# Performance work log

Hardware: AMD Instinct MI355X
Metric: run time of the kernel (lower is better)

Reference implementation:

```python
import jax, jax.numpy as jnp
from jax import lax
import numpy as np

EPS = 1e-8
NUM_ROUTES = 1152  # 32 * 6 * 6
NUM_OBJ = 10
OBJ_DIM = 16
PC_CAPS = 8
PC_CH = 32


def _squash(s, axis=-1):
    sq = jnp.sum(s * s, axis=axis, keepdims=True)
    return (sq / (1.0 + sq)) * s / jnp.sqrt(sq + EPS)


def setup_inputs() -> dict:
    key = jax.random.key(0)
    ks = jax.random.split(key, 12)
    B = 512
    image = jax.random.uniform(ks[0], (B, 1, 28, 28), dtype=jnp.float32)
    label = jax.random.randint(ks[1], (B,), 0, NUM_OBJ)
    conv_w = jax.random.normal(ks[2], (256, 1, 9, 9), dtype=jnp.float32) * 0.05
    conv_b = jnp.zeros((256,), jnp.float32)
    pc_w = jax.random.normal(ks[3], (PC_CAPS, PC_CH, 256, 9, 9), dtype=jnp.float32) * 0.02
    pc_b = jnp.zeros((PC_CAPS, PC_CH), jnp.float32)
    W_route = jax.random.normal(ks[4], (NUM_ROUTES, NUM_OBJ, OBJ_DIM, PC_CAPS), dtype=jnp.float32)
    dec_w1 = jax.random.normal(ks[5], (512, NUM_OBJ * OBJ_DIM), dtype=jnp.float32) * 0.05
    dec_b1 = jnp.zeros((512,), jnp.float32)
    dec_w2 = jax.random.normal(ks[6], (1024, 512), dtype=jnp.float32) * 0.05
    dec_b2 = jnp.zeros((1024,), jnp.float32)
    dec_w3 = jax.random.normal(ks[7], (784, 1024), dtype=jnp.float32) * 0.05
    dec_b3 = jnp.zeros((784,), jnp.float32)
    return {"image": image, "label": label, "conv_w": conv_w, "conv_b": conv_b,
            "pc_w": pc_w, "pc_b": pc_b, "W_route": W_route,
            "dec_w1": dec_w1, "dec_b1": dec_b1, "dec_w2": dec_w2, "dec_b2": dec_b2,
            "dec_w3": dec_w3, "dec_b3": dec_b3}


def reference(image, label, conv_w, conv_b, pc_w, pc_b, W_route,
              dec_w1, dec_b1, dec_w2, dec_b2, dec_w3, dec_b3):
    B = image.shape[0]
    # ConvEncoder: [B,1,28,28] -> [B,256,20,20]
    x = lax.conv_general_dilated(image, conv_w, (1, 1), 'VALID',
                                 dimension_numbers=('NCHW', 'OIHW', 'NCHW'))
    x = jax.nn.relu(x + conv_b[None, :, None, None])
    # PrimaryCaps: 8 parallel convs fused into one conv with 8*32 out channels
    pw = pc_w.reshape(PC_CAPS * PC_CH, 256, 9, 9)
    u = lax.conv_general_dilated(x, pw, (2, 2), 'VALID',
                                 dimension_numbers=('NCHW', 'OIHW', 'NCHW'))
    u = u + pc_b.reshape(-1)[None, :, None, None]  # [B,256,6,6] == stack dim=1 of [B,8,32,6,6]
    # faithful torch .view: [B,8,32,6,6] row-major -> [B,1152,8]
    u = u.reshape(B, NUM_ROUTES, PC_CAPS)
    u = _squash(u, axis=-1)
    # ObjectCaps dynamic routing
    # u_hat[b,r,j,o] = sum_c W[r,j,o,c] * u[b,r,c]
    u_hat = jnp.einsum('rjoc,brc->brjo', W_route, u)  # [B,1152,10,16]
    b_ij = jnp.zeros((B, NUM_ROUTES, NUM_OBJ), u_hat.dtype)
    v = None
    for it in range(3):
        c_ij = jax.nn.softmax(b_ij, axis=2)                  # softmax over capsules j
        s_j = jnp.einsum('brj,brjo->bjo', c_ij, u_hat)       # [B,10,16]
        v = _squash(s_j, axis=-1)
        if it < 2:
            b_ij = b_ij + jnp.einsum('brjo,bjo->brj', u_hat, v)
    obj_vectors = v[..., None]  # [B,10,16,1]
    # safe_norm over dim=2, squeeze(-1)
    y_prob = jnp.sqrt(jnp.sum(v * v, axis=-1) + EPS)  # [B,10]
    # Decoder: mask by label one-hot, MLP to reconstruction
    mask = jax.nn.one_hot(label, NUM_OBJ, dtype=v.dtype)
    masked = (v * mask[:, :, None]).reshape(B, NUM_OBJ * OBJ_DIM)
    h = jax.nn.relu(masked @ dec_w1.T + dec_b1)
    h = jax.nn.relu(h @ dec_w2.T + dec_b2)
    recon = jax.nn.sigmoid(h @ dec_w3.T + dec_b3).reshape(B, 1, 28, 28)
    return obj_vectors, recon, y_prob
```

## Files before the change

### kernel.cpp

```cpp
#include <hip/hip_runtime.h>
#include <hip/hip_bf16.h>

#define EPSF 1e-8f

typedef __attribute__((ext_vector_type(8))) short short8v;
typedef __attribute__((ext_vector_type(4))) float float4v;

static __device__ __forceinline__ unsigned short f2bf_bits(float x)
{
    return __builtin_bit_cast(unsigned short, __float2bfloat16(x));
}

__global__ __launch_bounds__(256) void k_prep(const float* __restrict__ pw,
                                              __hip_bfloat16* __restrict__ Bw2,
                                              const float* __restrict__ img,
                                              const float* __restrict__ cw,
                                              const float* __restrict__ cb,
                                              __hip_bfloat16* __restrict__ xt)
{
    __shared__ alignas(16) char shmem[41472];
    const int bid = blockIdx.x;
    const int t = threadIdx.x;

    if (bid < 256) {
        const int oc = bid;
        unsigned short* wl = (unsigned short*)shmem;
        for (int i = t; i < 20736; i += 256)
            wl[i] = f2bf_bits(pw[(size_t)oc * 20736 + i]);
        __syncthreads();
        const int r16 = oc & 15, nt = (oc >> 4) & 3, wcq = oc >> 6;
        for (int e = t; e < 2592; e += 256) {
            const int kidx = e >> 5, icc = (e >> 2) & 7, slot = e & 3;
            short8v v;
            #pragma unroll
            for (int i = 0; i < 8; ++i)
                v[i] = (short)wl[(icc * 32 + slot * 8 + i) * 81 + kidx];
            const int chunk = ((kidx * 8 + icc) * 4 + wcq) * 4 + nt;
            *(short8v*)(Bw2 + (size_t)chunk * 512 + (slot * 16 + r16) * 8) = v;
        }
        return;
    }

    const int b = bid - 256;
    const int c = t;
    float* simg = (float*)shmem;
    for (int i = c; i < 784; i += 256) simg[i] = img[b * 784 + i];
    float wreg[81];
    const float* wp = cw + c * 81;
    #pragma unroll
    for (int k = 0; k < 81; ++k) wreg[k] = wp[k];
    const float bias = cb[c];
    __syncthreads();

    const int icc = c >> 5, slot = (c >> 3) & 3, ic8 = c & 7;
    char* xbase = (char*)xt + ((size_t)b * 8 + icc) * 25600;

    for (int wg = 0; wg < 5; ++wg) {
        const float* base = &simg[wg * 4];
        float win[9][12];
        #pragma unroll
        for (int r = 0; r < 8; ++r) {
            const float4v* rp = (const float4v*)(base + r * 28);
            float4v A = rp[0], B = rp[1], C = rp[2];
            win[r][0] = A.x; win[r][1] = A.y; win[r][2]  = A.z; win[r][3]  = A.w;
            win[r][4] = B.x; win[r][5] = B.y; win[r][6]  = B.z; win[r][7]  = B.w;
            win[r][8] = C.x; win[r][9] = C.y; win[r][10] = C.z; win[r][11] = C.w;
        }
        #pragma unroll
        for (int h = 0; h < 20; ++h) {
            {
                const int ws = (h + 8) % 9;
                const float4v* rp = (const float4v*)(base + (h + 8) * 28);
                float4v A = rp[0], B = rp[1], C = rp[2];
                win[ws][0] = A.x; win[ws][1] = A.y; win[ws][2]  = A.z; win[ws][3]  = A.w;
                win[ws][4] = B.x; win[ws][5] = B.y; win[ws][6]  = B.z; win[ws][7]  = B.w;
                win[ws][8] = C.x; win[ws][9] = C.y; win[ws][10] = C.z; win[ws][11] = C.w;
            }
            float acc[4] = {bias, bias, bias, bias};
            #pragma unroll
            for (int ky = 0; ky < 9; ++ky) {
                const int rs = (h + ky) % 9;
                #pragma unroll
                for (int kx = 0; kx < 9; ++kx) {
                    const float wv = wreg[ky * 9 + kx];
                    #pragma unroll
                    for (int i = 0; i < 4; ++i)
                        acc[i] = fmaf(win[rs][kx + i], wv, acc[i]);
                }
            }
            #pragma unroll
            for (int i = 0; i < 4; ++i) {
                int w = wg * 4 + i;
                float av = fmaxf(acc[i], 0.f);
                int pos = h * 20 + (w & 1) * 10 + (w >> 1);
                int off = pos * 64 + ((slot ^ ((pos >> 1) & 3)) << 4) + ic8 * 2;
                *(unsigned short*)(xbase + off) = f2bf_bits(av);
            }
        }
    }
}

__device__ __forceinline__ void stage_x(const __hip_bfloat16* __restrict__ xt,
                                        char* dst, int b0, int icc, int t)
{
    const __hip_bfloat16* base0 = xt + ((size_t)(b0    ) * 8 + icc) * 12800;
    const __hip_bfloat16* base1 = xt + ((size_t)(b0 + 1) * 8 + icc) * 12800;
    #pragma unroll
    for (int k = 0; k < 12; ++k) {
        const int unit = t + k * 256;
        const __hip_bfloat16* gp = (unit < 1600) ? (base0 + unit * 8)
                                                 : (base1 + (unit - 1600) * 8);
        __builtin_amdgcn_global_load_lds(
            (const __attribute__((address_space(1))) unsigned int*)gp,
            (__attribute__((address_space(3))) unsigned int*)(dst + unit * 16),
            16, 0, 0);
    }
    if (t < 128) {
        const int unit = 3072 + t;
        const __hip_bfloat16* gp = base1 + (unit - 1600) * 8;
        __builtin_amdgcn_global_load_lds(
            (const __attribute__((address_space(1))) unsigned int*)gp,
            (__attribute__((address_space(3))) unsigned int*)(dst + unit * 16),
            16, 0, 0);
    }
}

__global__ __launch_bounds__(256, 2) void k_conv2(const __hip_bfloat16* __restrict__ xt,
                                                  const __hip_bfloat16* __restrict__ Bw2,
                                                  const float* __restrict__ pcb,
                                                  float* __restrict__ u0,
                                                  float* __restrict__ u1)
{
    const int pair = blockIdx.x >> 1;
    const int ks = blockIdx.x & 1;
    const int b0 = pair * 2;
    const int t = threadIdx.x;
    const int lane = t & 63, wc = t >> 6;
    const int r16 = lane & 15, slot = lane >> 4;

    __shared__ alignas(16) char xs[51200];

    int aimg[5], lc[5];
    #pragma unroll
    for (int mt = 0; mt < 5; ++mt) {
        int grow = mt * 16 + r16;
        int img = (grow >= 36 && grow < 72) ? 1 : 0;
        int hw = (grow < 72) ? (grow - 36 * img) : 0;
        int h = hw / 6, w = hw - h * 6;
        aimg[mt] = img * 25600;
        lc[mt] = 40 * h + w;
    }

    float4v acc[5][4];
    #pragma unroll
    for (int mt = 0; mt < 5; ++mt)
        #pragma unroll
        for (int nt = 0; nt < 4; ++nt)
            acc[mt][nt] = (float4v){0.f, 0.f, 0.f, 0.f};

    for (int i4 = 0; i4 < 4; ++i4) {
        const int icc = ks * 4 + i4;
        __syncthreads();
        stage_x(xt, xs, b0, icc, t);
        __syncthreads();

        const __hip_bfloat16* bp = Bw2 + ((size_t)icc * 4 + wc) * 2048 + lane * 8;

        #pragma unroll 3
        for (int kidx = 0; kidx < 81; ++kidx) {
            int ky = kidx / 9, kx = kidx - ky * 9;
            int scalK = 20 * ky + 10 * (kx & 1) + (kx >> 1);
            short8v a[5];
            #pragma unroll
            for (int mt = 0; mt < 5; ++mt) {
                int pos = lc[mt] + scalK;
                int off = aimg[mt] + pos * 64 + (((slot ^ (pos >> 1)) & 3) << 4);
                a[mt] = *(const short8v*)(xs + off);
            }
            const __hip_bfloat16* bq = bp + (size_t)kidx * 65536;
            short8v bv[4];
            #pragma unroll
            for (int nt = 0; nt < 4; ++nt)
                bv[nt] = *(const short8v*)(bq + nt * 512);
            #pragma unroll
            for (int mt = 0; mt < 5; ++mt)
                #pragma unroll
                for (int nt = 0; nt < 4; ++nt)
                    acc[mt][nt] = __builtin_amdgcn_mfma_f32_16x16x32_bf16(a[mt], bv[nt], acc[mt][nt], 0, 0, 0);
        }
    }

    float* uo = ks ? u1 : u0;
    #pragma unroll
    for (int mt = 0; mt < 5; ++mt) {
        int grow0 = mt * 16 + slot * 4;
        if (grow0 < 72) {
            int img = grow0 >= 36;
            int hwb = grow0 - 36 * img;
            const int b = b0 + img;
            #pragma unroll
            for (int nt = 0; nt < 4; ++nt) {
                int oc = wc * 64 + nt * 16 + r16;
                float pb = ks ? 0.f : pcb[oc];
                float4v v = acc[mt][nt];
                v.x += pb; v.y += pb; v.z += pb; v.w += pb;
                *(float4v*)(uo + (size_t)b * 9216 + oc * 36 + hwb) = v;
            }
        }
    }
}

__global__ __launch_bounds__(256, 2) void k_route3(const float* __restrict__ u0,
                                                   const float* __restrict__ u1,
                                                   const float* __restrict__ W,
                                                   const float* __restrict__ vsum,
                                                   float* __restrict__ spart, int iter)
{
    const int bid = blockIdx.x;
    const int rc = bid % 144;
    const int bc = bid / 144;
    const int r0 = rc * 8;
    const int b0 = bc * 128;
    const int t = threadIdx.x;
    const int oq = t & 3;
    const int img = t >> 2;
    const int bA = b0 + img, bB = bA + 64;

    __shared__ alignas(16) float Wl[10240];
    __shared__ alignas(16) float ul[128 * 68];

    #pragma unroll
    for (int k = 0; k < 10; ++k) {
        int e = t + k * 256;
        int rr = e / 320, rest = e - rr * 320;
        float4v val = *(const float4v*)(W + (size_t)(r0 + rr) * 1280 + rest * 4);
        int es = e ^ ((e >> 3) & 3);
        *(float4v*)(Wl + es * 4) = val;
    }
    #pragma unroll
    for (int k = 0; k < 4; ++k) {
        int e = t + k * 256;
        int im = e >> 3, cap = e & 7;
        size_t gb = (size_t)(b0 + im) * 9216 + rc * 64 + cap * 8;
        const float4v* pA = (const float4v*)(u0 + gb);
        const float4v* pB = (const float4v*)(u1 + gb);
        float4v a = pA[0] + pB[0];
        float4v c = pA[1] + pB[1];
        float sq = a.x * a.x + a.y * a.y + a.z * a.z + a.w * a.w
                 + c.x * c.x + c.y * c.y + c.z * c.z + c.w * c.w;
        float scale = (sq / (1.f + sq)) / sqrtf(sq + EPSF);
        a *= scale; c *= scale;
        *(float4v*)(ul + im * 68 + cap * 8) = a;
        *(float4v*)(ul + im * 68 + cap * 8 + 4) = c;
    }
    __syncthreads();

    float4v accA[10], accB[10];
    #pragma unroll
    for (int j = 0; j < 10; ++j) {
        accA[j] = (float4v){0.f, 0.f, 0.f, 0.f};
        accB[j] = (float4v){0.f, 0.f, 0.f, 0.f};
    }

    const float* upA = ul + img * 68;
    const float* upB = ul + (img + 64) * 68;

    for (int r = 0; r < 8; ++r) {
        float4v uA0 = *(const float4v*)(upA + r * 8);
        float4v uA1 = *(const float4v*)(upA + r * 8 + 4);
        float4v uB0 = *(const float4v*)(upB + r * 8);
        float4v uB1 = *(const float4v*)(upB + r * 8 + 4);
        float4v uhA[10], uhB[10];
        #pragma unroll
        for (int j = 0; j < 10; ++j) {
            #pragma unroll
            for (int oo = 0; oo < 4; ++oo) {
                int un = r * 320 + j * 32 + oq * 8 + oo * 2;
                int i0 = un ^ oq;
                int i1 = i0 ^ 1;
                float4v wlo = *(const float4v*)(Wl + i0 * 4);
                float4v whi = *(const float4v*)(Wl + i1 * 4);
                uhA[j][oo] = wlo.x * uA0.x + wlo.y * uA0.y + wlo.z * uA0.z + wlo.w * uA0.w
                           + whi.x * uA1.x + whi.y * uA1.y + whi.z * uA1.z + whi.w * uA1.w;
                uhB[j][oo] = wlo.x * uB0.x + wlo.y * uB0.y + wlo.z * uB0.z + wlo.w * uB0.w
                           + whi.x * uB1.x + whi.y * uB1.y + whi.z * uB1.z + whi.w * uB1.w;
            }
        }
        if (iter > 0) {
            #pragma unroll 2
            for (int half = 0; half < 2; ++half) {
                const int b = half ? bB : bA;
                float4v* uh = half ? uhB : uhA;
                float4v* acc = half ? accB : accA;
                float q[10];
                #pragma unroll
                for (int j = 0; j < 10; ++j) {
                    float4v vj = *(const float4v*)(vsum + (size_t)b * 160 + j * 16 + oq * 4);
                    float qp = uh[j].x * vj.x + uh[j].y * vj.y
                             + uh[j].z * vj.z + uh[j].w * vj.w;
                    qp += __shfl_xor(qp, 1);
                    qp += __shfl_xor(qp, 2);
                    q[j] = qp;
                }
                float mx = q[0];
                #pragma unroll
                for (int j = 1; j < 10; ++j) mx = fmaxf(mx, q[j]);
                float ssum = 0.f;
                float c[10];
                #pragma unroll
                for (int j = 0; j < 10; ++j) { c[j] = __expf(q[j] - mx); ssum += c[j]; }
                float inv = 1.f / ssum;
                #pragma unroll
                for (int j = 0; j < 10; ++j) acc[j] += (c[j] * inv) * uh[j];
            }
        } else {
            #pragma unroll
            for (int j = 0; j < 10; ++j) {
                accA[j] += 0.1f * uhA[j];
                accB[j] += 0.1f * uhB[j];
            }
        }
    }

    float* dstA = spart + ((size_t)rc * 512 + bA) * 160 + oq * 4;
    float* dstB = spart + ((size_t)rc * 512 + bB) * 160 + oq * 4;
    #pragma unroll
    for (int j = 0; j < 10; ++j) {
        *(float4v*)(dstA + j * 16) = accA[j];
        *(float4v*)(dstB + j * 16) = accB[j];
    }
}

__global__ void k_finish(const float* __restrict__ spart, float* __restrict__ vsum,
                         float* __restrict__ obj, float* __restrict__ yprob, int iter)
{
    const int b = blockIdx.x, t = threadIdx.x;
    if (t < 160) {
        const float* sp = spart + (size_t)b * 160 + t;
        float sv = 0.f;
        #pragma unroll 8
        for (int rc = 0; rc < 144; ++rc)
            sv += sp[(size_t)rc * 81920];
        float sq = sv * sv;
        sq += __shfl_xor(sq, 1); sq += __shfl_xor(sq, 2);
        sq += __shfl_xor(sq, 4); sq += __shfl_xor(sq, 8);
        float v = sv * (sq / (1.f + sq)) / sqrtf(sq + EPSF);
        float pv = (iter > 0) ? vsum[b * 160 + t] : 0.f;
        vsum[b * 160 + t] = pv + v;
        if (iter == 2) {
            obj[b * 160 + t] = v;
            float vv = v * v;
            vv += __shfl_xor(vv, 1); vv += __shfl_xor(vv, 2);
            vv += __shfl_xor(vv, 4); vv += __shfl_xor(vv, 8);
            if ((t & 15) == 0) yprob[b * 10 + (t >> 4)] = sqrtf(vv + EPSF);
        }
    }
}

__global__ __launch_bounds__(256) void k_mlp1g(const float* __restrict__ obj,
                                               const int* __restrict__ label,
                                               const float* __restrict__ w1,
                                               const float* __restrict__ b1,
                                               float* __restrict__ h1)
{
    const int b0 = blockIdx.x * 8;
    const int t = threadIdx.x;
    __shared__ float vl[8][16];
    __shared__ int labs[8];
    if (t < 8) labs[t] = label[b0 + t];
    __syncthreads();
    if (t < 128) {
        int m = t >> 4, o = t & 15;
        vl[m][o] = obj[(size_t)(b0 + m) * 160 + labs[m] * 16 + o];
    }
    __syncthreads();
    #pragma unroll 2
    for (int nn = 0; nn < 2; ++nn) {
        const int n = t + nn * 256;
        const float bs = b1[n];
        #pragma unroll
        for (int m = 0; m < 8; ++m) {
            const float4v* wp = (const float4v*)(w1 + (size_t)n * 160 + labs[m] * 16);
            float4v w0 = wp[0], w1v = wp[1], w2 = wp[2], w3 = wp[3];
            float q = bs;
            q += vl[m][0]  * w0.x  + vl[m][1]  * w0.y  + vl[m][2]  * w0.z  + vl[m][3]  * w0.w;
            q += vl[m][4]  * w1v.x + vl[m][5]  * w1v.y + vl[m][6]  * w1v.z + vl[m][7]  * w1v.w;
            q += vl[m][8]  * w2.x  + vl[m][9]  * w2.y  + vl[m][10] * w2.z  + vl[m][11] * w2.w;
            q += vl[m][12] * w3.x  + vl[m][13] * w3.y  + vl[m][14] * w3.z  + vl[m][15] * w3.w;
            h1[(size_t)(b0 + m) * 512 + n] = fmaxf(q, 0.f);
        }
    }
}

__global__ void k_mlp(const float* __restrict__ A, const float* __restrict__ Wt,
                      const float* __restrict__ bias, float* __restrict__ C,
                      int N, int K, int act)
{
    const int m0 = blockIdx.x * 32;
    const int n0 = blockIdx.y * 32;
    const int t  = threadIdx.x;
    const int tn = t & 31, tg = t >> 5;
    __shared__ float As[32][33];
    __shared__ float Ws[32][33];
    float acc[4] = {0.f, 0.f, 0.f, 0.f};
    for (int k0 = 0; k0 < K; k0 += 32) {
        __syncthreads();
        for (int idx = t; idx < 1024; idx += 256) {
            int rr = idx >> 5, kk = idx & 31;
            As[rr][kk] = A[(size_t)(m0 + rr) * K + k0 + kk];
            int n = n0 + rr;
            Ws[rr][kk] = (n < N) ? Wt[(size_t)n * K + k0 + kk] : 0.f;
        }
        __syncthreads();
        #pragma unroll 8
        for (int kk = 0; kk < 32; ++kk) {
            float bv = Ws[tn][kk];
            #pragma unroll
            for (int i = 0; i < 4; ++i)
                acc[i] += As[tg * 4 + i][kk] * bv;
        }
    }
    int n = n0 + tn;
    if (n < N) {
        float bs = bias[n];
        #pragma unroll
        for (int i = 0; i < 4; ++i) {
            float vv = acc[i] + bs;
            vv = (act == 0) ? fmaxf(vv, 0.f) : 1.f / (1.f + expf(-vv));
            C[(size_t)(m0 + tg * 4 + i) * N + n] = vv;
        }
    }
}

extern "C" void kernel_launch(void* const* d_in, const int* in_sizes, int n_in,
                              void* d_out, int out_size, void* d_ws, size_t ws_size,
                              hipStream_t stream)
{
    const float* image  = (const float*)d_in[0];
    const int*   label  = (const int*)  d_in[1];
    const float* conv_w = (const float*)d_in[2];
    const float* conv_b = (const float*)d_in[3];
    const float* pc_w   = (const float*)d_in[4];
    const float* pc_b   = (const float*)d_in[5];
    const float* Wrt    = (const float*)d_in[6];
    const float* dw1 = (const float*)d_in[7];
    const float* db1 = (const float*)d_in[8];
    const float* dw2 = (const float*)d_in[9];
    const float* db2 = (const float*)d_in[10];
    const float* dw3 = (const float*)d_in[11];
    const float* db3 = (const float*)d_in[12];
    float* out = (float*)d_out;

    char* p = (char*)d_ws;
    __hip_bfloat16* xt  = (__hip_bfloat16*)p; p += 104857600;
    float* u      = (float*)p; p += 18874368;
    float* u1     = (float*)p; p += 18874368;
    __hip_bfloat16* Bw2 = (__hip_bfloat16*)p; p += 10616832;
    float* vsum   = (float*)p; p += 327680;
    float* h1     = (float*)p; p += 1048576;
    float* h2     = (float*)p; p += 2097152;

    float* spart = (float*)xt;

    float* obj   = out;
    float* recon = out + 81920;
    float* yprob = out + 483328;

    k_prep<<<768, 256, 0, stream>>>(pc_w, Bw2, image, conv_w, conv_b, xt);
    k_conv2<<<512, 256, 0, stream>>>(xt, Bw2, pc_b, u, u1);
    for (int it = 0; it < 3; ++it) {
        k_route3<<<576, 256, 0, stream>>>(u, u1, Wrt, vsum, spart, it);
        k_finish<<<512, 192, 0, stream>>>(spart, vsum, obj, yprob, it);
    }
    k_mlp1g<<<64, 256, 0, stream>>>(obj, label, dw1, db1, h1);
    k_mlp<<<dim3(16, 32), 256, 0, stream>>>(h1, dw2, db2, h2, 1024, 512, 0);
    k_mlp<<<dim3(16, 25), 256, 0, stream>>>(h2, dw3, db3, recon, 784, 1024, 1);
}
```

Before: 681.0 us.

## Compute first conv layer with bf16 MFMA im2col instead of scalar FMA

Replaces the per-thread scalar FMA sliding-window 9x9 convolution in the prep kernel with an im2col formulation on bf16 MFMA 16x16x32 instructions. The image and conv weights are staged in LDS as bf16 with K padded to 96, and each wave computes tiles of 16 output positions by 256 channels. This is meant to cut the ALU cost of the first conv. In exchange it lowers input and weight precision to bf16, uses more LDS per block, and writes output with scattered stores.

New measurement: 635.9 us (median of 2 runs). 6.6% less time.

```diff
diff --git a/kernel.cpp b/kernel.cpp
--- a/kernel.cpp
+++ b/kernel.cpp
@@ -18,7 +18,7 @@
                                               const float* __restrict__ cb,
                                               __hip_bfloat16* __restrict__ xt)
 {
-    __shared__ alignas(16) char shmem[41472];
+    __shared__ alignas(16) char shmem[54016];
     const int bid = blockIdx.x;
     const int t = threadIdx.x;
 
@@ -42,59 +42,66 @@
     }
 
     const int b = bid - 256;
-    const int c = t;
-    float* simg = (float*)shmem;
-    for (int i = c; i < 784; i += 256) simg[i] = img[b * 784 + i];
-    float wreg[81];
-    const float* wp = cw + c * 81;
-    #pragma unroll
-    for (int k = 0; k < 81; ++k) wreg[k] = wp[k];
-    const float bias = cb[c];
+    const int lane = t & 63, wid = t >> 6;
+    const int r16 = lane & 15, slot = lane >> 4;
+
+    unsigned short* simgbf = (unsigned short*)shmem;
+    int* offT             = (int*)(shmem + 3200);
+    unsigned short* Bw1c  = (unsigned short*)(shmem + 3584);
+    float* cbl            = (float*)(shmem + 52928);
+
+    for (int i = t; i < 784; i += 256) simgbf[i] = f2bf_bits(img[b * 784 + i]);
+    for (int i = 784 + t; i < 1600; i += 256) simgbf[i] = 0;
+    if (t < 96) offT[t] = (t < 81) ? (t / 9) * 28 + (t % 9) : 1000;
+    cbl[t] = cb[t];
+    for (int e = t; e < 3072; e += 256) {
+        const int chunk = e >> 8, c = e & 255;
+        #pragma unroll
+        for (int i = 0; i < 8; ++i) {
+            const int k = chunk * 8 + i;
+            Bw1c[chunk * 2056 + c * 8 + i] =
+                (k < 81) ? f2bf_bits(cw[c * 81 + k]) : (unsigned short)0;
+        }
+    }
     __syncthreads();
 
-    const int icc = c >> 5, slot = (c >> 3) & 3, ic8 = c & 7;
-    char* xbase = (char*)xt + ((size_t)b * 8 + icc) * 25600;
-
-    for (int wg = 0; wg < 5; ++wg) {
-        const float* base = &simg[wg * 4];
-        float win[9][12];
-        #pragma unroll
-        for (int r = 0; r < 8; ++r) {
-            const float4v* rp = (const float4v*)(base + r * 28);
-            float4v A = rp[0], B = rp[1], C = rp[2];
-            win[r][0] = A.x; win[r][1] = A.y; win[r][2]  = A.z; win[r][3]  = A.w;
-            win[r][4] = B.x; win[r][5] = B.y; win[r][6]  = B.z; win[r][7]  = B.w;
-            win[r][8] = C.x; win[r][9] = C.y; win[r][10] = C.z; win[r][11] = C.w;
-        }
-        #pragma unroll
-        for (int h = 0; h < 20; ++h) {
-            {
-                const int ws = (h + 8) % 9;
-                const float4v* rp = (const float4v*)(base + (h + 8) * 28);
-                float4v A = rp[0], B = rp[1], C = rp[2];
-                win[ws][0] = A.x; win[ws][1] = A.y; win[ws][2]  = A.z; win[ws][3]  = A.w;
-                win[ws][4] = B.x; win[ws][5] = B.y; win[ws][6]  = B.z; win[ws][7]  = B.w;
-                win[ws][8] = C.x; win[ws][9] = C.y; win[ws][10] = C.z; win[ws][11] = C.w;
-            }
-            float acc[4] = {bias, bias, bias, bias};
-            #pragma unroll
-            for (int ky = 0; ky < 9; ++ky) {
-                const int rs = (h + ky) % 9;
-                #pragma unroll
-                for (int kx = 0; kx < 9; ++kx) {
-                    const float wv = wreg[ky * 9 + kx];
-                    #pragma unroll
-                    for (int i = 0; i < 4; ++i)
-                        acc[i] = fmaf(win[rs][kx + i], wv, acc[i]);
-                }
-            }
+    char* xb = (char*)xt + (size_t)b * 8 * 25600;
+
+    for (int m = wid; m < 25; m += 4) {
+        const int pos_r = m * 16 + r16;
+        const int hh = (pos_r * 3277) >> 16;
+        const int ww = pos_r - hh * 20;
+        const int abase = hh * 28 + ww;
+        short8v a[3];
+        #pragma unroll
+        for (int ks = 0; ks < 3; ++ks) {
+            #pragma unroll
+            for (int i = 0; i < 8; ++i) {
+                const int k = ks * 32 + slot * 8 + i;
+                a[ks][i] = (short)simgbf[abase + offT[k]];
+            }
+        }
+        #pragma unroll 4
+        for (int nt = 0; nt < 16; ++nt) {
+            float4v acc4 = (float4v){0.f, 0.f, 0.f, 0.f};
+            #pragma unroll
+            for (int ks = 0; ks < 3; ++ks) {
+                short8v bv = *(const short8v*)(Bw1c + (ks * 4 + slot) * 2056
+                                               + (nt * 16 + r16) * 8);
+                acc4 = __builtin_amdgcn_mfma_f32_16x16x32_bf16(a[ks], bv, acc4, 0, 0, 0);
+            }
+            const int c = nt * 16 + r16;
+            const int icc_ = c >> 5, sl = (c >> 3) & 3, i8 = c & 7;
+            const float cbv = cbl[c];
+            char* xc = xb + icc_ * 25600 + i8 * 2;
             #pragma unroll
             for (int i = 0; i < 4; ++i) {
-                int w = wg * 4 + i;
-                float av = fmaxf(acc[i], 0.f);
-                int pos = h * 20 + (w & 1) * 10 + (w >> 1);
-                int off = pos * 64 + ((slot ^ ((pos >> 1) & 3)) << 4) + ic8 * 2;
-                *(unsigned short*)(xbase + off) = f2bf_bits(av);
+                const int pos = m * 16 + slot * 4 + i;
+                const int h2 = (pos * 3277) >> 16;
+                const int w2 = pos - h2 * 20;
+                const int pp = h2 * 20 + (w2 & 1) * 10 + (w2 >> 1);
+                const float v = fmaxf(acc4[i] + cbv, 0.f);
+                *(unsigned short*)(xc + pp * 64 + ((sl ^ ((pp >> 1) & 3)) << 4)) = f2bf_bits(v);
             }
         }
     }
```
